# Kernel optimization log

Hardware: AMD Instinct MI355X
Metric: run time of the kernel (lower is better)

The kernel has to match this reference:

```python
import jax, jax.numpy as jnp
import numpy as np

D, H, S, L = 512, 8, 4, 2
HD = D // H          # 64 head dim
F = 4 * D            # 2048 FFN hidden
EPS = 1e-5


def setup_inputs() -> dict:
    key = jax.random.key(0)
    ks = jax.random.split(key, 26)
    B = 16384
    w = 0.02
    inp = {
        'text_pattern':   jax.random.normal(ks[0], (B, D), jnp.float32),
        'text_semantic':  jax.random.normal(ks[1], (B, D), jnp.float32),
        'image_pattern':  jax.random.normal(ks[2], (B, D), jnp.float32),
        'image_semantic': jax.random.normal(ks[3], (B, D), jnp.float32),
        # per-(layer, stream) attention projections, stacked [L,S,...]
        'Wq': jax.random.normal(ks[4], (L, S, D, D), jnp.float32) * w,
        'bq': jnp.zeros((L, S, D), jnp.float32),
        'Wk': jax.random.normal(ks[5], (L, S, D, D), jnp.float32) * w,
        'bk': jnp.zeros((L, S, D), jnp.float32),
        'Wv': jax.random.normal(ks[6], (L, S, D, D), jnp.float32) * w,
        'bv': jnp.zeros((L, S, D), jnp.float32),
        'Wo': jax.random.normal(ks[7], (L, S, D, D), jnp.float32) * w,
        'bo': jnp.zeros((L, S, D), jnp.float32),
        'ln_g': jnp.ones((L, S, D), jnp.float32),
        'ln_b': jnp.zeros((L, S, D), jnp.float32),
        'W1': jax.random.normal(ks[8], (L, S, D, F), jnp.float32) * w,
        'b1': jnp.zeros((L, S, F), jnp.float32),
        'W2': jax.random.normal(ks[9], (L, S, F, D), jnp.float32) * w,
        'b2': jnp.zeros((L, S, D), jnp.float32),
        # final fusion MLP: 4*D -> 2*D -> D
        'Wf1': jax.random.normal(ks[10], (S * D, 2 * D), jnp.float32) * w,
        'bf1': jnp.zeros((2 * D,), jnp.float32),
        'Wf2': jax.random.normal(ks[11], (2 * D, D), jnp.float32) * w,
        'bf2': jnp.zeros((D,), jnp.float32),
    }
    return inp


def _layer_norm(x, g, b):
    # x: [B,S,D], g/b: [S,D]; normalize over last dim
    mu = jnp.mean(x, axis=-1, keepdims=True)
    var = jnp.mean(jnp.square(x - mu), axis=-1, keepdims=True)
    return (x - mu) * jax.lax.rsqrt(var + EPS) * g + b


def reference(text_pattern, text_semantic, image_pattern, image_semantic,
              Wq, bq, Wk, bk, Wv, bv, Wo, bo, ln_g, ln_b,
              W1, b1, W2, b2, Wf1, bf1, Wf2, bf2):
    # streams stacked: [B, S=4, D]; each stream's query_len is 1, keys are all 4 streams
    x = jnp.stack([text_pattern, text_semantic, image_pattern, image_semantic], axis=1)
    B = x.shape[0]
    attn0 = None
    for l in range(L):
        # per-stream query projection of its own token: [B,S,D]
        q = jnp.einsum('bsd,sde->bse', x, Wq[l]) + bq[l]
        # per-stream K/V projections of ALL streams: [B,S(query-stream),K(key-pos),D]
        k = jnp.einsum('bkd,sde->bske', x, Wk[l]) + bk[l][:, None, :]
        v = jnp.einsum('bkd,sde->bske', x, Wv[l]) + bv[l][:, None, :]
        qh = q.reshape(B, S, H, HD)
        kh = k.reshape(B, S, S, H, HD)
        vh = v.reshape(B, S, S, H, HD)
        scores = jnp.einsum('bshe,bskhe->bshk', qh, kh) / (HD ** 0.5)  # [B,S,H,K]
        w = jax.nn.softmax(scores, axis=-1)
        ctx = jnp.einsum('bshk,bskhe->bshe', w, vh).reshape(B, S, D)
        attn_out = jnp.einsum('bsd,sde->bse', ctx, Wo[l]) + bo[l]
        if l == 0:
            attn0 = w  # [B,S,H,K]: layer-0 attention weights per stream
        h = _layer_norm(x + attn_out, ln_g[l], ln_b[l])
        ffn = jnp.einsum('bsf,sfd->bsd',
                         jax.nn.relu(jnp.einsum('bsd,sdf->bsf', h, W1[l]) + b1[l]),
                         W2[l]) + b2[l]
        x = h + ffn
    concat = x.reshape(B, S * D)
    fused = jax.nn.relu(concat @ Wf1 + bf1) @ Wf2 + bf2  # [B, D]
    return fused, attn0
```

## Files before the change

kernel.cpp:

```cpp
#include <hip/hip_runtime.h>
#include <stdint.h>

typedef unsigned short u16;
typedef __bf16 bf16x8 __attribute__((ext_vector_type(8)));
typedef float f32x4 __attribute__((ext_vector_type(4)));

constexpr int NB = 16384;
constexpr int DM = 512;
constexpr int NS = 4;
constexpr int FH = 2048;
constexpr int XW = NS * DM;
constexpr float EPSL = 1e-5f;

__device__ __forceinline__ float bf2f(u16 u) { return __uint_as_float(((uint32_t)u) << 16); }
__device__ __forceinline__ u16 f2bf(float f) {
  uint32_t u = __float_as_uint(f);
  u += 0x7fffu + ((u >> 16) & 1u);
  return (u16)(u >> 16);
}
__device__ __forceinline__ void unpack8(uint4 p, float* f) {
  f[0] = __uint_as_float(p.x << 16); f[1] = __uint_as_float(p.x & 0xffff0000u);
  f[2] = __uint_as_float(p.y << 16); f[3] = __uint_as_float(p.y & 0xffff0000u);
  f[4] = __uint_as_float(p.z << 16); f[5] = __uint_as_float(p.z & 0xffff0000u);
  f[6] = __uint_as_float(p.w << 16); f[7] = __uint_as_float(p.w & 0xffff0000u);
}
__device__ __forceinline__ uint4 pack8(const float* f) {
  uint4 r;
  r.x = (uint32_t)f2bf(f[0]) | ((uint32_t)f2bf(f[1]) << 16);
  r.y = (uint32_t)f2bf(f[2]) | ((uint32_t)f2bf(f[3]) << 16);
  r.z = (uint32_t)f2bf(f[4]) | ((uint32_t)f2bf(f[5]) << 16);
  r.w = (uint32_t)f2bf(f[6]) | ((uint32_t)f2bf(f[7]) << 16);
  return r;
}
__device__ __forceinline__ void gl_lds16(const void* g, void* l) {
  __builtin_amdgcn_global_load_lds((const __attribute__((address_space(1))) void*)g,
                                   (__attribute__((address_space(3))) void*)l, 16, 0, 0);
}

__device__ __forceinline__ void remap(int& bx, int& by, int& bz) {
  const int gx = gridDim.x, gy = gridDim.y;
  const int fl = (blockIdx.z * gy + blockIdx.y) * gx + blockIdx.x;
  const int xcd = fl & 7;
  const int t = fl >> 3;
  const int bw = gx >> 3;
  bx = xcd * bw + t % bw;
  const int u = t / bw;
  by = u % gy;
  bz = u / gy;
}

__device__ __forceinline__ void gemm_cv(
    const u16* __restrict__ A, int lda,
    const u16* __restrict__ Bt, int K,
    u16* As, u16* Bs, f32x4 (&acc)[4][4], int bx, int by)
{
  const int tid = threadIdx.x;
  const int ln = tid & 63;
  const int w  = tid >> 6;
  const int wm = w >> 1, wn = w & 1;
  const int m0 = bx * 128;
  const int n0 = by * 128;
  const int grow = ln >> 2;
  const int gcol = ((ln & 3) ^ ((ln >> 3) & 3)) * 8;
  const u16* Ab = A  + (size_t)(m0 + w * 32 + grow) * lda + gcol;
  const u16* Bb = Bt + (size_t)(n0 + w * 32 + grow) * K   + gcol;

  auto stage = [&](int buf, int k0) {
#pragma unroll
    for (int i = 0; i < 2; ++i) {
      gl_lds16(Ab + (size_t)i * 16 * lda + k0, &As[buf * 4096 + (w * 32 + i * 16) * 32]);
      gl_lds16(Bb + (size_t)i * 16 * K   + k0, &Bs[buf * 4096 + (w * 32 + i * 16) * 32]);
    }
  };

  __syncthreads();
  const int nt = K >> 5;
  stage(0, 0);
  if (nt > 1) {
    stage(1, 32);
    asm volatile("s_waitcnt vmcnt(4)" ::: "memory");
  } else {
    asm volatile("s_waitcnt vmcnt(0)" ::: "memory");
  }
  __builtin_amdgcn_s_barrier();
  asm volatile("" ::: "memory");

  const int rx = ((ln & 15) >> 1) & 3;
  const int qb = ln >> 4;
  const int cb = (qb ^ rx) * 8;
  int cur = 0, nxt2 = 2;
  for (int t = 0; t < nt; ++t) {
    bf16x8 af[4], bfv[4];
#pragma unroll
    for (int m = 0; m < 4; ++m) {
      af[m]  = *(const bf16x8*)&As[cur * 4096 + (wm * 64 + m * 16 + (ln & 15)) * 32 + cb];
      bfv[m] = *(const bf16x8*)&Bs[cur * 4096 + (wn * 64 + m * 16 + (ln & 15)) * 32 + cb];
    }
#pragma unroll
    for (int m = 0; m < 4; ++m)
#pragma unroll
      for (int n = 0; n < 4; ++n)
        acc[m][n] = __builtin_amdgcn_mfma_f32_16x16x32_bf16(af[m], bfv[n], acc[m][n], 0, 0, 0);
    if (t + 2 < nt) {
      stage(nxt2, (t + 2) * 32);
      asm volatile("s_waitcnt vmcnt(4)" ::: "memory");
      __builtin_amdgcn_s_barrier();
      asm volatile("" ::: "memory");
    } else if (t + 1 < nt) {
      asm volatile("s_waitcnt vmcnt(0)" ::: "memory");
      __builtin_amdgcn_s_barrier();
      asm volatile("" ::: "memory");
    }
    cur = cur + 1;  if (cur == 3)  cur = 0;
    nxt2 = nxt2 + 1; if (nxt2 == 3) nxt2 = 0;
  }
  asm volatile("" ::: "memory");
}

template<bool RELU, bool RESID, bool OUTF32>
__global__ __launch_bounds__(256) void k_gemm(
    const u16* __restrict__ A, int lda, long aZ,
    const u16* __restrict__ Bt, long bZ,
    const float* __restrict__ bias, long biasZ,
    const u16* __restrict__ Rsd, int ldr, long rZ,
    void* __restrict__ Cp, int ldc, long cZ, int K)
{
  int bx, by, bz; remap(bx, by, bz);
  A += (long)bz * aZ; Bt += (long)bz * bZ; bias += (long)bz * biasZ;
  __shared__ alignas(16) u16 As[3 * 4096];
  __shared__ alignas(16) u16 Bs[3 * 4096];
  f32x4 acc[4][4] = {};
  gemm_cv(A, lda, Bt, K, As, Bs, acc, bx, by);
  const int ln = threadIdx.x & 63;
  const int w = threadIdx.x >> 6;
  const int wm = w >> 1, wn = w & 1;
  const int m0 = bx * 128, n0 = by * 128;
#pragma unroll
  for (int n = 0; n < 4; ++n) {
    const int gc = n0 + wn * 64 + n * 16 + (ln & 15);
    const float bv = bias[gc];
#pragma unroll
    for (int m = 0; m < 4; ++m) {
#pragma unroll
      for (int j = 0; j < 4; ++j) {
        const int gr = m0 + wm * 64 + m * 16 + (ln >> 4) * 4 + j;
        float v = acc[m][n][j] + bv;
        if constexpr (RESID) v += bf2f(Rsd[(long)bz * rZ + (size_t)gr * ldr + gc]);
        if constexpr (RELU)  v = v > 0.f ? v : 0.f;
        if constexpr (OUTF32) ((float*)Cp)[(long)bz * cZ + (size_t)gr * ldc + gc] = v;
        else                  ((u16*)Cp)[(long)bz * cZ + (size_t)gr * ldc + gc] = f2bf(v);
      }
    }
  }
}

__global__ __launch_bounds__(256) void k_kdot(
    const u16* __restrict__ xcat, const u16* __restrict__ WkT_l,
    const u16* __restrict__ Qb, float* __restrict__ wbuf)
{
  int bx, by, kp; remap(bx, by, kp);
  __shared__ alignas(16) u16 As[3 * 4096];
  __shared__ alignas(16) u16 Bs[3 * 4096];
  f32x4 acc[4][4] = {};
  gemm_cv(xcat + kp * DM, XW, WkT_l, DM, As, Bs, acc, bx, by);
  const int ln = threadIdx.x & 63;
  const int w = threadIdx.x >> 6;
  const int wm = w >> 1, wn = w & 1;
  const int m0 = bx * 128, n0 = by * 128;
  const int colbase = n0 + wn * 64;
  const int s = colbase >> 9;
  const int h = (colbase >> 6) & 7;
  float p[4][4];
#pragma unroll
  for (int m = 0; m < 4; ++m)
#pragma unroll
    for (int j = 0; j < 4; ++j) p[m][j] = 0.f;
#pragma unroll
  for (int n = 0; n < 4; ++n) {
    const int qc = (colbase & 511) + n * 16 + (ln & 15);
#pragma unroll
    for (int m = 0; m < 4; ++m) {
#pragma unroll
      for (int j = 0; j < 4; ++j) {
        const int gr = m0 + wm * 64 + m * 16 + (ln >> 4) * 4 + j;
        p[m][j] += acc[m][n][j] * bf2f(Qb[((size_t)s * NB + gr) * DM + qc]);
      }
    }
  }
#pragma unroll
  for (int m = 0; m < 4; ++m)
#pragma unroll
    for (int j = 0; j < 4; ++j) {
      float v = p[m][j];
      v += __shfl_xor(v, 1, 64);
      v += __shfl_xor(v, 2, 64);
      v += __shfl_xor(v, 4, 64);
      v += __shfl_xor(v, 8, 64);
      p[m][j] = v;
    }
  if ((ln & 15) == 0) {
#pragma unroll
    for (int m = 0; m < 4; ++m)
#pragma unroll
      for (int j = 0; j < 4; ++j) {
        const int gr = m0 + wm * 64 + m * 16 + (ln >> 4) * 4 + j;
        wbuf[(((size_t)s * NB + gr) * 8 + h) * 4 + kp] = p[m][j] * 0.125f;
      }
  }
}

__global__ __launch_bounds__(256) void k_gemmv4(
    const u16* __restrict__ xcat, const u16* __restrict__ WvT_l,
    const float* __restrict__ bv_l, const float* __restrict__ wbuf,
    u16* __restrict__ ctxc)
{
  int bx, by, bz; remap(bx, by, bz); (void)bz;
  __shared__ alignas(16) u16 As[3 * 4096];
  __shared__ alignas(16) u16 Bs[3 * 4096];
  const int ln = threadIdx.x & 63;
  const int w = threadIdx.x >> 6;
  const int wm = w >> 1, wn = w & 1;
  const int m0 = bx * 128, n0 = by * 128;
  const int s  = n0 >> 9;
  const int hh = ((n0 >> 6) + wn) & 7;
  f32x4 facc[4][4] = {};
  for (int kp = 0; kp < 4; ++kp) {
    f32x4 acc[4][4] = {};
    gemm_cv(xcat + kp * DM, XW, WvT_l, DM, As, Bs, acc, bx, by);
    float wv[4][4];
#pragma unroll
    for (int m = 0; m < 4; ++m)
#pragma unroll
      for (int j = 0; j < 4; ++j) {
        const int gr = m0 + wm * 64 + m * 16 + (ln >> 4) * 4 + j;
        wv[m][j] = wbuf[(((size_t)s * NB + gr) * 8 + hh) * 4 + kp];
      }
#pragma unroll
    for (int n = 0; n < 4; ++n) {
      const float bvv = bv_l[n0 + wn * 64 + n * 16 + (ln & 15)];
#pragma unroll
      for (int m = 0; m < 4; ++m)
#pragma unroll
        for (int j = 0; j < 4; ++j)
          facc[m][n][j] += (acc[m][n][j] + bvv) * wv[m][j];
    }
  }
#pragma unroll
  for (int n = 0; n < 4; ++n) {
    const int gc = n0 + wn * 64 + n * 16 + (ln & 15);
#pragma unroll
    for (int m = 0; m < 4; ++m)
#pragma unroll
      for (int j = 0; j < 4; ++j) {
        const int gr = m0 + wm * 64 + m * 16 + (ln >> 4) * 4 + j;
        ctxc[(size_t)gr * XW + gc] = f2bf(facc[m][n][j]);
      }
  }
}

__global__ __launch_bounds__(256) void k_softmax(
    float* __restrict__ wbuf, float* __restrict__ a0)
{
  const int t = blockIdx.x * 256 + threadIdx.x;
  float4 v = ((const float4*)wbuf)[t];
  const float mx = fmaxf(fmaxf(v.x, v.y), fmaxf(v.z, v.w));
  float4 e;
  e.x = __expf(v.x - mx); e.y = __expf(v.y - mx);
  e.z = __expf(v.z - mx); e.w = __expf(v.w - mx);
  const float inv = 1.f / (e.x + e.y + e.z + e.w);
  e.x *= inv; e.y *= inv; e.z *= inv; e.w *= inv;
  ((float4*)wbuf)[t] = e;
  if (a0 != nullptr) {
    const int s = t >> 17, b = (t >> 3) & (NB - 1), h = t & 7;
    ((float4*)a0)[((size_t)b * NS + s) * 8 + h] = e;
  }
}

__global__ __launch_bounds__(256) void k_ln(
    u16* __restrict__ xcat, const float* __restrict__ g, const float* __restrict__ bb)
{
  const int ln = threadIdx.x & 63;
  const int row = blockIdx.x * 4 + (threadIdx.x >> 6);
  const int b = row >> 2, s = row & 3;
  u16* p = xcat + (size_t)b * XW + s * DM;
  float v[8];
  { uint4 t = ((const uint4*)p)[ln]; unpack8(t, v); }
  float sum = 0.f;
#pragma unroll
  for (int j = 0; j < 8; ++j) sum += v[j];
#pragma unroll
  for (int off = 1; off < 64; off <<= 1) sum += __shfl_xor(sum, off, 64);
  const float mu = sum * (1.f / DM);
  float s2 = 0.f;
#pragma unroll
  for (int j = 0; j < 8; ++j) { float d = v[j] - mu; s2 += d * d; }
#pragma unroll
  for (int off = 1; off < 64; off <<= 1) s2 += __shfl_xor(s2, off, 64);
  const float rs = rsqrtf(s2 * (1.f / DM) + EPSL);
  const int e0 = s * DM + ln * 8;
  float o[8];
#pragma unroll
  for (int j = 0; j < 8; ++j) o[j] = (v[j] - mu) * rs * g[e0 + j] + bb[e0 + j];
  ((uint4*)p)[ln] = pack8(o);
}

__global__ void k_pack(const float* __restrict__ t0, const float* __restrict__ t1,
                       const float* __restrict__ t2, const float* __restrict__ t3,
                       u16* __restrict__ xcat)
{
  const int total = NB * XW / 8;
  for (int t = blockIdx.x * blockDim.x + threadIdx.x; t < total; t += gridDim.x * blockDim.x) {
    const int b = t >> 8;
    const int r = t & 255;
    const int s = r >> 6;
    const int d0 = (r & 63) * 8;
    const float* p = (s == 0) ? t0 : (s == 1) ? t1 : (s == 2) ? t2 : t3;
    float f[8];
#pragma unroll
    for (int j = 0; j < 8; ++j) f[j] = p[(size_t)b * DM + d0 + j];
    ((uint4*)xcat)[t] = pack8(f);
  }
}

__global__ __launch_bounds__(256) void k_tcvt(
    const float* __restrict__ src, u16* __restrict__ dst, int R, int C)
{
  __shared__ float tl[32][33];
  const int cx = blockIdx.x * 32, ry = blockIdx.y * 32;
  const size_t base = (size_t)blockIdx.z * R * C;
  const int lx = threadIdx.x & 31, ly = threadIdx.x >> 5;
#pragma unroll
  for (int i = 0; i < 32; i += 8)
    tl[ly + i][lx] = src[base + (size_t)(ry + ly + i) * C + cx + lx];
  __syncthreads();
#pragma unroll
  for (int i = 0; i < 32; i += 8)
    dst[base + (size_t)(cx + ly + i) * R + ry + lx] = f2bf(tl[lx][ly + i]);
}

extern "C" void kernel_launch(void* const* d_in, const int* in_sizes, int n_in,
                              void* d_out, int out_size, void* d_ws, size_t ws_size,
                              hipStream_t stream)
{
  (void)in_sizes; (void)n_in; (void)out_size;
  const float* t0  = (const float*)d_in[0];
  const float* t1  = (const float*)d_in[1];
  const float* t2  = (const float*)d_in[2];
  const float* t3  = (const float*)d_in[3];
  const float* Wq  = (const float*)d_in[4];
  const float* bq  = (const float*)d_in[5];
  const float* Wk  = (const float*)d_in[6];
  const float* Wv  = (const float*)d_in[8];
  const float* bv  = (const float*)d_in[9];
  const float* Wo  = (const float*)d_in[10];
  const float* bo  = (const float*)d_in[11];
  const float* lng = (const float*)d_in[12];
  const float* lnb = (const float*)d_in[13];
  const float* W1  = (const float*)d_in[14];
  const float* b1  = (const float*)d_in[15];
  const float* W2  = (const float*)d_in[16];
  const float* b2  = (const float*)d_in[17];
  const float* Wf1 = (const float*)d_in[18];
  const float* bf1 = (const float*)d_in[19];
  const float* Wf2 = (const float*)d_in[20];
  const float* bf2 = (const float*)d_in[21];

  size_t off = 0;
  char* ws = (char*)d_ws;
  auto take = [&](size_t n) { char* p = ws + off; off += (n + 255) & ~(size_t)255; return p; };
  u16* WqT  = (u16*)take(8ull * DM * DM * 2);
  u16* WkT  = (u16*)take(8ull * DM * DM * 2);
  u16* WvT  = (u16*)take(8ull * DM * DM * 2);
  u16* WoT  = (u16*)take(8ull * DM * DM * 2);
  u16* W1T  = (u16*)take(8ull * DM * FH * 2);
  u16* W2T  = (u16*)take(8ull * FH * DM * 2);
  u16* Wf1T = (u16*)take((size_t)XW * 1024 * 2);
  u16* Wf2T = (u16*)take((size_t)1024 * DM * 2);
  u16* xcat = (u16*)take((size_t)NB * XW * 2);
  char* U1  = take((size_t)NB * XW * 2);
  float* wbuf = (float*)take(4ull * NB * 8 * 4 * 4);
  const size_t needed = off;

  u16* Qb   = (u16*)U1;
  u16* ctxc = (u16*)U1;
  u16* ffn1 = (u16*)U1;
  u16* y1   = (u16*)U1;
  float* attn0 = (float*)d_out + (size_t)NB * DM;

  if (needed > ws_size) return;

  k_tcvt<<<dim3(16, 16, 8), dim3(256), 0, stream>>>(Wq, WqT, DM, DM);
  k_tcvt<<<dim3(16, 16, 8), dim3(256), 0, stream>>>(Wk, WkT, DM, DM);
  k_tcvt<<<dim3(16, 16, 8), dim3(256), 0, stream>>>(Wv, WvT, DM, DM);
  k_tcvt<<<dim3(16, 16, 8), dim3(256), 0, stream>>>(Wo, WoT, DM, DM);
  k_tcvt<<<dim3(64, 16, 8), dim3(256), 0, stream>>>(W1, W1T, DM, FH);
  k_tcvt<<<dim3(16, 64, 8), dim3(256), 0, stream>>>(W2, W2T, FH, DM);
  k_tcvt<<<dim3(32, 64, 1), dim3(256), 0, stream>>>(Wf1, Wf1T, XW, 1024);
  k_tcvt<<<dim3(16, 32, 1), dim3(256), 0, stream>>>(Wf2, Wf2T, 1024, DM);
  k_pack<<<dim3(2048), dim3(256), 0, stream>>>(t0, t1, t2, t3, xcat);

  const long WSQ = (long)DM * DM;
  for (int ly = 0; ly < 2; ++ly) {
    const u16* WqT_l = WqT + (size_t)ly * 4 * WSQ;
    const u16* WkT_l = WkT + (size_t)ly * 4 * WSQ;
    const u16* WvT_l = WvT + (size_t)ly * 4 * WSQ;
    const u16* WoT_l = WoT + (size_t)ly * 4 * WSQ;
    k_gemm<false, false, false><<<dim3(128, 4, 4), dim3(256), 0, stream>>>(
        xcat, XW, DM, WqT_l, WSQ, bq + (size_t)ly * XW, DM,
        nullptr, 0, 0, Qb, DM, (long)NB * DM, DM);
    k_kdot<<<dim3(128, 16, 4), dim3(256), 0, stream>>>(xcat, WkT_l, Qb, wbuf);
    k_softmax<<<dim3(4 * NB * 8 / 256), dim3(256), 0, stream>>>(
        wbuf, (ly == 0) ? attn0 : (float*)nullptr);
    k_gemmv4<<<dim3(128, 16), dim3(256), 0, stream>>>(
        xcat, WvT_l, bv + (size_t)ly * XW, wbuf, ctxc);
    k_gemm<false, true, false><<<dim3(128, 4, 4), dim3(256), 0, stream>>>(
        ctxc, XW, DM, WoT_l, WSQ, bo + (size_t)ly * XW, DM,
        xcat, XW, DM, xcat, XW, DM, DM);
    k_ln<<<dim3(NB), dim3(256), 0, stream>>>(xcat, lng + ly * XW, lnb + ly * XW);
    for (int s = 0; s < NS; ++s) {
      const size_t wsl = (size_t)(ly * 4 + s);
      k_gemm<true, false, false><<<dim3(128, 16, 1), dim3(256), 0, stream>>>(
          xcat + s * DM, XW, 0, W1T + wsl * (size_t)DM * FH, 0, b1 + wsl * FH, 0,
          nullptr, 0, 0, ffn1, FH, 0, DM);
      k_gemm<false, true, false><<<dim3(128, 4, 1), dim3(256), 0, stream>>>(
          ffn1, FH, 0, W2T + wsl * (size_t)FH * DM, 0, b2 + wsl * DM, 0,
          xcat + s * DM, XW, 0, xcat + s * DM, XW, 0, FH);
    }
  }
  k_gemm<true, false, false><<<dim3(128, 8, 1), dim3(256), 0, stream>>>(
      xcat, XW, 0, Wf1T, 0, bf1, 0, nullptr, 0, 0, y1, 1024, 0, XW);
  k_gemm<false, false, true><<<dim3(128, 4, 1), dim3(256), 0, stream>>>(
      y1, 1024, 0, Wf2T, 0, bf2, 0, nullptr, 0, 0, d_out, DM, 0, 1024);
}
```

Measured before the change: 2.445 ms.

## Mix inputs by attention weights before V projection instead of after

The V-context kernel now forms the attention-weighted sum of the four stream inputs per head first, then runs a single GEMM against Wv, replacing four separate GEMMs whose outputs were weighted and accumulated. This relies on linearity, since softmax weights sum to one and the bias is added once. The goal is to cut the V-path MFMA work by roughly four. It adds a custom double-buffered loop with register A loads, on-the-fly bf16 mixing, and global-to-LDS B loads, and the mixed inputs are rounded to bf16 before the matmul.

```diff
diff --git a/kernel.cpp b/kernel.cpp
--- a/kernel.cpp
+++ b/kernel.cpp
@@ -31,6 +31,11 @@
   r.z = (uint32_t)f2bf(f[4]) | ((uint32_t)f2bf(f[5]) << 16);
   r.w = (uint32_t)f2bf(f[6]) | ((uint32_t)f2bf(f[7]) << 16);
   return r;
+}
+__device__ __forceinline__ uint32_t cvtpk(float lo, float hi) {
+  uint32_t d;
+  asm("v_cvt_pk_bf16_f32 %0, %1, %2" : "=v"(d) : "v"(lo), "v"(hi));
+  return d;
 }
 __device__ __forceinline__ void gl_lds16(const void* g, void* l) {
   __builtin_amdgcn_global_load_lds((const __attribute__((address_space(1))) void*)g,
@@ -209,52 +214,118 @@
   }
 }
 
-__global__ __launch_bounds__(256) void k_gemmv4(
+__global__ __launch_bounds__(256) void k_gemmvm(
     const u16* __restrict__ xcat, const u16* __restrict__ WvT_l,
     const float* __restrict__ bv_l, const float* __restrict__ wbuf,
     u16* __restrict__ ctxc)
 {
   int bx, by, bz; remap(bx, by, bz); (void)bz;
-  __shared__ alignas(16) u16 As[3 * 4096];
-  __shared__ alignas(16) u16 Bs[3 * 4096];
-  const int ln = threadIdx.x & 63;
-  const int w = threadIdx.x >> 6;
+  __shared__ alignas(16) u16 Am[2 * 8192];
+  __shared__ alignas(16) u16 Bsh[2 * 4096];
+  const int tid = threadIdx.x;
+  const int ln = tid & 63;
+  const int w  = tid >> 6;
   const int wm = w >> 1, wn = w & 1;
-  const int m0 = bx * 128, n0 = by * 128;
+  const int m0 = bx * 128;
+  const int n0 = by * 128;
   const int s  = n0 >> 9;
-  const int hh = ((n0 >> 6) + wn) & 7;
-  f32x4 facc[4][4] = {};
-  for (int kp = 0; kp < 4; ++kp) {
-    f32x4 acc[4][4] = {};
-    gemm_cv(xcat + kp * DM, XW, WvT_l, DM, As, Bs, acc, bx, by);
-    float wv[4][4];
+  const int h0 = (n0 >> 6) & 7;
+  const int lr = ln & 15;
+  const int kq = (ln >> 4) * 8;
+  const u16* Abase = xcat  + (size_t)(m0 + w * 32 + lr) * XW + kq;
+  const u16* Bbase = WvT_l + (size_t)(n0 + w * 32 + lr) * DM + kq;
+
+  float4 wg[2][2];
+#pragma unroll
+  for (int i = 0; i < 2; ++i) {
+    const int r = m0 + (w * 2 + i) * 16 + lr;
+#pragma unroll
+    for (int j = 0; j < 2; ++j)
+      wg[i][j] = *(const float4*)&wbuf[(((size_t)s * NB + r) * 8 + h0 + j) * 4];
+  }
+
+  uint4 ar[2][4];
+  auto loadA = [&](int k0) {
+#pragma unroll
+    for (int i = 0; i < 2; ++i)
+#pragma unroll
+      for (int kp = 0; kp < 4; ++kp)
+        ar[i][kp] = *(const uint4*)(Abase + (size_t)i * 16 * XW + kp * DM + k0);
+  };
+  auto loadB = [&](int buf, int k0) {
+#pragma unroll
+    for (int i = 0; i < 2; ++i)
+      gl_lds16(Bbase + (size_t)i * 16 * DM + k0,
+               &Bsh[buf * 4096 + (w * 2 + i) * 512 + ln * 8]);
+  };
+  auto mixwrite = [&](int buf) {
+#pragma unroll
+    for (int i = 0; i < 2; ++i) {
+      float x[4][8];
+#pragma unroll
+      for (int kp = 0; kp < 4; ++kp) unpack8(ar[i][kp], x[kp]);
+#pragma unroll
+      for (int j = 0; j < 2; ++j) {
+        const float4 g = wg[i][j];
+        float o[8];
+#pragma unroll
+        for (int e = 0; e < 8; ++e)
+          o[e] = g.x * x[0][e] + g.y * x[1][e] + g.z * x[2][e] + g.w * x[3][e];
+        uint4 pk;
+        pk.x = cvtpk(o[0], o[1]); pk.y = cvtpk(o[2], o[3]);
+        pk.z = cvtpk(o[4], o[5]); pk.w = cvtpk(o[6], o[7]);
+        *(uint4*)&Am[buf * 8192 + ((j * 8) + (w * 2 + i)) * 512 + ln * 8] = pk;
+      }
+    }
+  };
+
+  f32x4 acc[4][4] = {};
+  const int nt = DM / 32;
+
+  loadA(0); loadB(0, 0);
+  asm volatile("s_waitcnt vmcnt(0)" ::: "memory");
+  mixwrite(0);
+  asm volatile("s_waitcnt lgkmcnt(0)" ::: "memory");
+  __builtin_amdgcn_s_barrier();
+  asm volatile("" ::: "memory");
+
+  int cbuf = 0;
+  for (int t = 0; t < nt; ++t) {
+    if (t + 1 < nt) { loadA((t + 1) * 32); loadB(cbuf ^ 1, (t + 1) * 32); }
+    bf16x8 af[4], bfv[4];
 #pragma unroll
     for (int m = 0; m < 4; ++m)
+      af[m] = *(const bf16x8*)&Am[cbuf * 8192 + (wn * 8 + wm * 4 + m) * 512 + ln * 8];
+#pragma unroll
+    for (int n = 0; n < 4; ++n)
+      bfv[n] = *(const bf16x8*)&Bsh[cbuf * 4096 + (wn * 4 + n) * 512 + ln * 8];
+#pragma unroll
+    for (int m = 0; m < 4; ++m)
+#pragma unroll
+      for (int n = 0; n < 4; ++n)
+        acc[m][n] = __builtin_amdgcn_mfma_f32_16x16x32_bf16(af[m], bfv[n], acc[m][n], 0, 0, 0);
+    if (t + 1 < nt) {
+      asm volatile("s_waitcnt vmcnt(0)" ::: "memory");
+      mixwrite(cbuf ^ 1);
+      asm volatile("s_waitcnt lgkmcnt(0)" ::: "memory");
+      __builtin_amdgcn_s_barrier();
+      asm volatile("" ::: "memory");
+      cbuf ^= 1;
+    }
+  }
+
+#pragma unroll
+  for (int nf = 0; nf < 4; ++nf) {
+    const int gc = n0 + wn * 64 + nf * 16 + (ln & 15);
+    const float bvv = bv_l[gc];
+#pragma unroll
+    for (int mf = 0; mf < 4; ++mf) {
 #pragma unroll
       for (int j = 0; j < 4; ++j) {
-        const int gr = m0 + wm * 64 + m * 16 + (ln >> 4) * 4 + j;
-        wv[m][j] = wbuf[(((size_t)s * NB + gr) * 8 + hh) * 4 + kp];
+        const int gr = m0 + wm * 64 + mf * 16 + (ln >> 4) * 4 + j;
+        ctxc[(size_t)gr * XW + gc] = f2bf(acc[mf][nf][j] + bvv);
       }
-#pragma unroll
-    for (int n = 0; n < 4; ++n) {
-      const float bvv = bv_l[n0 + wn * 64 + n * 16 + (ln & 15)];
-#pragma unroll
-      for (int m = 0; m < 4; ++m)
-#pragma unroll
-        for (int j = 0; j < 4; ++j)
-          facc[m][n][j] += (acc[m][n][j] + bvv) * wv[m][j];
-    }
-  }
-#pragma unroll
-  for (int n = 0; n < 4; ++n) {
-    const int gc = n0 + wn * 64 + n * 16 + (ln & 15);
-#pragma unroll
-    for (int m = 0; m < 4; ++m)
-#pragma unroll
-      for (int j = 0; j < 4; ++j) {
-        const int gr = m0 + wm * 64 + m * 16 + (ln >> 4) * 4 + j;
-        ctxc[(size_t)gr * XW + gc] = f2bf(facc[m][n][j]);
-      }
+    }
   }
 }
 
@@ -411,7 +482,7 @@
     k_kdot<<<dim3(128, 16, 4), dim3(256), 0, stream>>>(xcat, WkT_l, Qb, wbuf);
     k_softmax<<<dim3(4 * NB * 8 / 256), dim3(256), 0, stream>>>(
         wbuf, (ly == 0) ? attn0 : (float*)nullptr);
-    k_gemmv4<<<dim3(128, 16), dim3(256), 0, stream>>>(
+    k_gemmvm<<<dim3(128, 16), dim3(256), 0, stream>>>(
         xcat, WvT_l, bv + (size_t)ly * XW, wbuf, ctxc);
     k_gemm<false, true, false><<<dim3(128, 4, 4), dim3(256), 0, stream>>>(
         ctxc, XW, DM, WoT_l, WSQ, bo + (size_t)ly * XW, DM,
```

New measurement: 2.249 ms. -8.0%, faster.
